# Performance work log

Measured on AMD Instinct MI355X. Metric: run time of the kernel, lower is better.

Reference implementation:

```python
import jax, jax.numpy as jnp
import numpy as np

D_MODEL = 1024
N_HEADS = 16
D_Q = 64
D_V = 64
N_SEG = 16
EPS_LN = 1e-5
EPS_MEM = 1e-6


def setup_inputs() -> dict:
    key = jax.random.key(0)
    ks = jax.random.split(key, 10)
    N, T = 4, 4096
    inp = {
        "query_sequences": jax.random.normal(ks[0], (N, T, D_MODEL), dtype=jnp.float32),
        "key_sequences": jax.random.normal(ks[1], (N, T, D_MODEL), dtype=jnp.float32),
        "value_sequences": jax.random.normal(ks[2], (N, T, D_MODEL), dtype=jnp.float32),
        "Wq": jax.random.normal(ks[3], (D_MODEL, N_HEADS * D_Q), dtype=jnp.float32) * 0.02,
        "Wk": jax.random.normal(ks[4], (D_MODEL, N_HEADS * D_Q), dtype=jnp.float32) * 0.02,
        "Wv": jax.random.normal(ks[5], (D_MODEL, N_HEADS * D_V), dtype=jnp.float32) * 0.02,
        "Wo": jax.random.normal(ks[6], (N_HEADS * D_V, D_MODEL), dtype=jnp.float32) * 0.02,
        "ln_w": jnp.ones((D_MODEL,), dtype=jnp.float32),
        "ln_b": jnp.zeros((D_MODEL,), dtype=jnp.float32),
        "beta": jnp.ones((1,), dtype=jnp.float32),
    }
    return inp


def _layer_norm(x, w, b):
    mu = jnp.mean(x, axis=-1, keepdims=True)
    var = jnp.var(x, axis=-1, keepdims=True)
    return (x - mu) * jax.lax.rsqrt(var + EPS_LN) * w + b


def reference(query_sequences, key_sequences, value_sequences, Wq, Wk, Wv, Wo, ln_w, ln_b, beta):
    N, t, _ = query_sequences.shape
    S = t // N_SEG  # segment length (256)

    # qkv_norm applied to q, and (self-attention) to k and v as well
    qn = _layer_norm(query_sequences, ln_w, ln_b)
    kn = _layer_norm(key_sequences, ln_w, ln_b)
    vn = _layer_norm(value_sequences, ln_w, ln_b)

    # project and split heads -> [N, H, t, d]
    qh = (qn @ Wq).reshape(N, t, N_HEADS, D_Q).transpose(0, 2, 1, 3)
    kh = (kn @ Wk).reshape(N, t, N_HEADS, D_Q).transpose(0, 2, 1, 3)
    vh = (vn @ Wv).reshape(N, t, N_HEADS, D_V).transpose(0, 2, 1, 3)

    # segment: [N_SEG, N, H, S, d] so lax.scan iterates segments sequentially
    seg = lambda x, d: x.reshape(N, N_HEADS, N_SEG, S, d).transpose(2, 0, 1, 3, 4)
    q_segs, k_segs, v_segs = seg(qh, D_Q), seg(kh, D_Q), seg(vh, D_V)

    b_gate = jax.nn.sigmoid(beta)[0]            # scalar mixing gate
    scale = 1.0 / np.sqrt(D_Q).astype(np.float32)
    causal = jnp.tril(jnp.ones((S, S), dtype=bool))

    def step(carry, xs):
        mem, z = carry                          # [N,H,Dq,Dv], [N,H,Dq]
        qs, ks_, vs = xs                        # [N,H,S,d]
        sq = jax.nn.elu(qs) + 1.0
        sk = jax.nn.elu(ks_) + 1.0
        # retrieve from compressive memory
        num = jnp.einsum('nhsd,nhde->nhse', sq, mem)
        den = jnp.einsum('nhsd,nhd->nhs', sq, z)[..., None] + EPS_MEM
        a_mem = num / den                       # [N,H,S,Dv]
        # local causal softmax attention within the segment
        scores = jnp.einsum('nhsd,nhtd->nhst', qs, ks_) * scale
        scores = jnp.where(causal, scores, -jnp.inf)
        probs = jax.nn.softmax(scores, axis=-1)
        attn = jnp.einsum('nhst,nhtd->nhsd', probs, vs)
        out = b_gate * a_mem + (1.0 - b_gate) * attn
        # linear memory update
        mem = mem + jnp.einsum('nhsd,nhse->nhde', sk, vs)
        z = z + sk.sum(axis=2)
        return (mem, z), out

    mem0 = jnp.zeros((N, N_HEADS, D_Q, D_V), dtype=query_sequences.dtype)
    z0 = jnp.zeros((N, N_HEADS, D_Q), dtype=query_sequences.dtype)
    _, outs = jax.lax.scan(step, (mem0, z0), (q_segs, k_segs, v_segs))

    # outs: [N_SEG, N, H, S, Dv] -> [N, t, H*Dv]
    seqs = outs.transpose(1, 0, 3, 2, 4).reshape(N, t, N_HEADS * D_V)
    return seqs @ Wo
```

## Files before the change

kernel.cpp:

```cpp
#include <hip/hip_runtime.h>
#include <stdint.h>
#include <math.h>


typedef __attribute__((ext_vector_type(8))) short bf16x8_t;
typedef __attribute__((ext_vector_type(4))) short short4_t;
typedef __attribute__((ext_vector_type(4))) float f32x4;

__device__ __forceinline__ float bf2f(short s){
  union { unsigned u; float f; } v; v.u = ((unsigned)(unsigned short)s) << 16; return v.f;
}
__device__ __forceinline__ short f2bf(float f){
  union { float fl; unsigned u; } v; v.fl = f;
  unsigned r = v.u + 0x7FFFu + ((v.u >> 16) & 1u);
  return (short)(unsigned short)(r >> 16);
}
__device__ __forceinline__ f32x4 mfma16(bf16x8_t a, bf16x8_t b, f32x4 c){
  return __builtin_amdgcn_mfma_f32_16x16x32_bf16(a, b, c, 0, 0, 0);
}
__device__ __forceinline__ void gl_lds16(const short* g, short* l){
  __builtin_amdgcn_global_load_lds((const __attribute__((address_space(1))) void*)g,
                                   (__attribute__((address_space(3))) void*)l, 16, 0, 0);
}

__global__ __launch_bounds__(256) void ln3(const float* __restrict__ xq, const float* __restrict__ xk,
                                           const float* __restrict__ xv,
                                           const float* __restrict__ gw, const float* __restrict__ gb,
                                           short* __restrict__ oq, short* __restrict__ ok,
                                           short* __restrict__ ov){
  const int row = blockIdx.x, which = blockIdx.y, tid = threadIdx.x;
  const float* x = which == 0 ? xq : which == 1 ? xk : xv;
  short* out     = which == 0 ? oq : which == 1 ? ok : ov;
  const float4 v = *reinterpret_cast<const float4*>(x + (size_t)row*1024 + tid*4);
  float s  = v.x + v.y + v.z + v.w;
  float s2 = v.x*v.x + v.y*v.y + v.z*v.z + v.w*v.w;
  #pragma unroll
  for (int off = 1; off < 64; off <<= 1){
    s  += __shfl_xor(s,  off);
    s2 += __shfl_xor(s2, off);
  }
  __shared__ float red[8];
  if ((tid & 63) == 0){ red[tid>>6] = s; red[4 + (tid>>6)] = s2; }
  __syncthreads();
  s  = red[0] + red[1] + red[2] + red[3];
  s2 = red[4] + red[5] + red[6] + red[7];
  const float mu  = s * (1.0f/1024.0f);
  const float var = s2 * (1.0f/1024.0f) - mu*mu;
  const float rs  = rsqrtf(var + 1e-5f);
  const float4 wv = *reinterpret_cast<const float4*>(gw + tid*4);
  const float4 bv = *reinterpret_cast<const float4*>(gb + tid*4);
  short4_t o;
  o[0] = f2bf((v.x-mu)*rs*wv.x + bv.x);
  o[1] = f2bf((v.y-mu)*rs*wv.y + bv.y);
  o[2] = f2bf((v.z-mu)*rs*wv.z + bv.z);
  o[3] = f2bf((v.w-mu)*rs*wv.w + bv.w);
  *reinterpret_cast<short4_t*>(out + (size_t)row*1024 + tid*4) = o;
}

__global__ __launch_bounds__(256) void wcast4(const float* __restrict__ W0, const float* __restrict__ W1,
                                              const float* __restrict__ W2, const float* __restrict__ W3,
                                              short* __restrict__ T0, short* __restrict__ T1,
                                              short* __restrict__ T2, short* __restrict__ T3){
  const int z = blockIdx.z;
  const float* W = z == 0 ? W0 : z == 1 ? W1 : z == 2 ? W2 : W3;
  short* Wt      = z == 0 ? T0 : z == 1 ? T1 : z == 2 ? T2 : T3;
  __shared__ float tile[64][65];
  const int bx = blockIdx.x, by = blockIdx.y, tid = threadIdx.x;
  #pragma unroll
  for (int p=0;p<4;++p){
    int idx = p*256 + tid;
    int r = idx >> 4, c4 = (idx & 15) << 2;
    const float4 v = *reinterpret_cast<const float4*>(W + (size_t)(by*64 + r)*1024 + bx*64 + c4);
    tile[r][c4+0] = v.x; tile[r][c4+1] = v.y; tile[r][c4+2] = v.z; tile[r][c4+3] = v.w;
  }
  __syncthreads();
  #pragma unroll
  for (int p=0;p<4;++p){
    int idx = p*256 + tid;
    int r = idx >> 4, c4 = (idx & 15) << 2;
    short4_t o;
    o[0] = f2bf(tile[c4+0][r]); o[1] = f2bf(tile[c4+1][r]);
    o[2] = f2bf(tile[c4+2][r]); o[3] = f2bf(tile[c4+3][r]);
    *reinterpret_cast<short4_t*>(Wt + (size_t)(bx*64 + r)*1024 + by*64 + c4) = o;
  }
}

__device__ __forceinline__ void remap_mc(int n, int& m0, int& c0){
  int xcd = n & 7, idx = n >> 3;
  m0 = ((xcd << 3) + (idx & 7)) << 8;
  c0 = (idx >> 3) << 8;
}

__device__ __forceinline__ void gemm_body(short* smem, const short* __restrict__ A,
                                          const short* __restrict__ Bt, void* __restrict__ C,
                                          int mode, int m0, int c0){
  short* As = smem;
  short* Bs = smem + 32768;
  const int tid = threadIdx.x;
  const int lane = tid & 63, wid = tid >> 6;
  const int wr = wid >> 2, wc = wid & 3;
  const int l15 = lane & 15, lhi = lane >> 4;

  const short* Asrc[4]; const short* Bsrc[4];
  #pragma unroll
  for (int p=0;p<4;++p){
    int i = tid + 512*p;
    int r = i >> 3, g = (i & 7) ^ (r & 7);
    Asrc[p] = A  + (size_t)(m0 + r)*1024 + g*8;
    Bsrc[p] = Bt + (size_t)(c0 + r)*1024 + g*8;
  }

  f32x4 acc[8][4];
  #pragma unroll
  for (int m=0;m<8;++m)
    #pragma unroll
    for (int n=0;n<4;++n) acc[m][n] = (f32x4){0.f,0.f,0.f,0.f};

  #define STAGE_A0(t) { short* _d=&As[((t)&1)<<14]; int _k=(t)<<6; \
      gl_lds16(Asrc[0]+_k, _d+tid*8); gl_lds16(Asrc[1]+_k, _d+4096+tid*8); }
  #define STAGE_A1(t) { short* _d=&As[((t)&1)<<14]; int _k=(t)<<6; \
      gl_lds16(Asrc[2]+_k, _d+8192+tid*8); gl_lds16(Asrc[3]+_k, _d+12288+tid*8); }
  #define STAGE_B0(t) { short* _d=&Bs[((t)&1)<<14]; int _k=(t)<<6; \
      gl_lds16(Bsrc[0]+_k, _d+tid*8); gl_lds16(Bsrc[1]+_k, _d+4096+tid*8); }
  #define STAGE_B1(t) { short* _d=&Bs[((t)&1)<<14]; int _k=(t)<<6; \
      gl_lds16(Bsrc[2]+_k, _d+8192+tid*8); gl_lds16(Bsrc[3]+_k, _d+12288+tid*8); }

  STAGE_B0(0); STAGE_A0(0); STAGE_B1(0); STAGE_A1(0);
  STAGE_B0(1); STAGE_A0(1);
  asm volatile("s_waitcnt vmcnt(4)" ::: "memory");
  __builtin_amdgcn_s_barrier();

  for (int t = 0; t < 16; ++t){
    const short* Ab = &As[(t & 1) << 14];
    const short* Bb = &Bs[(t & 1) << 14];
    bf16x8_t af[4][2], bfr[4][2];
    #pragma unroll
    for (int m=0;m<4;++m){
      int r = wr*128 + m*16 + l15;
      #pragma unroll
      for (int ks=0;ks<2;++ks){
        int sl = (ks*4 + lhi) ^ (r & 7);
        af[m][ks] = *reinterpret_cast<const bf16x8_t*>(&Ab[r*64 + sl*8]);
      }
    }
    #pragma unroll
    for (int n=0;n<2;++n){
      int r = wc*64 + n*16 + l15;
      #pragma unroll
      for (int ks=0;ks<2;++ks){
        int sl = (ks*4 + lhi) ^ (r & 7);
        bfr[n][ks] = *reinterpret_cast<const bf16x8_t*>(&Bb[r*64 + sl*8]);
      }
    }
    if (t < 15) STAGE_B1(t+1);
    __builtin_amdgcn_s_setprio(1);
    #pragma unroll
    for (int m=0;m<4;++m)
      #pragma unroll
      for (int n=0;n<2;++n)
        #pragma unroll
        for (int ks=0;ks<2;++ks)
          acc[m][n] = mfma16(af[m][ks], bfr[n][ks], acc[m][n]);
    __builtin_amdgcn_s_setprio(0);
    #pragma unroll
    for (int n=2;n<4;++n){
      int r = wc*64 + n*16 + l15;
      #pragma unroll
      for (int ks=0;ks<2;++ks){
        int sl = (ks*4 + lhi) ^ (r & 7);
        bfr[n][ks] = *reinterpret_cast<const bf16x8_t*>(&Bb[r*64 + sl*8]);
      }
    }
    if (t < 15) STAGE_A1(t+1);
    __builtin_amdgcn_s_setprio(1);
    #pragma unroll
    for (int m=0;m<4;++m)
      #pragma unroll
      for (int n=2;n<4;++n)
        #pragma unroll
        for (int ks=0;ks<2;++ks)
          acc[m][n] = mfma16(af[m][ks], bfr[n][ks], acc[m][n]);
    __builtin_amdgcn_s_setprio(0);
    asm volatile("" ::: "memory");
    __builtin_amdgcn_s_barrier();
    asm volatile("" ::: "memory");
    #pragma unroll
    for (int m=0;m<4;++m){
      int r = wr*128 + 64 + m*16 + l15;
      #pragma unroll
      for (int ks=0;ks<2;++ks){
        int sl = (ks*4 + lhi) ^ (r & 7);
        af[m][ks] = *reinterpret_cast<const bf16x8_t*>(&Ab[r*64 + sl*8]);
      }
    }
    if (t < 14) STAGE_B0(t+2);
    __builtin_amdgcn_s_setprio(1);
    #pragma unroll
    for (int m=0;m<4;++m)
      #pragma unroll
      for (int n=0;n<2;++n)
        #pragma unroll
        for (int ks=0;ks<2;++ks)
          acc[4+m][n] = mfma16(af[m][ks], bfr[n][ks], acc[4+m][n]);
    __builtin_amdgcn_s_setprio(0);
    asm volatile("" ::: "memory");
    __builtin_amdgcn_s_barrier();
    asm volatile("" ::: "memory");
    if (t < 14) STAGE_A0(t+2);
    __builtin_amdgcn_s_setprio(1);
    #pragma unroll
    for (int m=0;m<4;++m)
      #pragma unroll
      for (int n=2;n<4;++n)
        #pragma unroll
        for (int ks=0;ks<2;++ks)
          acc[4+m][n] = mfma16(af[m][ks], bfr[n][ks], acc[4+m][n]);
    __builtin_amdgcn_s_setprio(0);
    if (t < 14)       { asm volatile("s_waitcnt vmcnt(4)" ::: "memory"); }
    else if (t == 14) { asm volatile("s_waitcnt vmcnt(0)" ::: "memory"); }
    if (t < 15) __builtin_amdgcn_s_barrier();
  }
  #undef STAGE_A0
  #undef STAGE_A1
  #undef STAGE_B0
  #undef STAGE_B1

  if (mode == 0){
    short* Cb = (short*)C;
    #pragma unroll
    for (int m=0;m<8;++m)
      #pragma unroll
      for (int n=0;n<4;++n)
        #pragma unroll
        for (int j=0;j<4;++j){
          int row = m0 + wr*128 + m*16 + lhi*4 + j;
          int col = c0 + wc*64 + n*16 + l15;
          size_t oidx = ((size_t)((row>>12)*16 + (col>>6)) * 4096 + (size_t)(row & 4095)) * 64 + (col & 63);
          Cb[oidx] = f2bf(acc[m][n][j]);
        }
  } else if (mode == 2){
    short* Cb = (short*)C;
    #pragma unroll
    for (int m=0;m<8;++m)
      #pragma unroll
      for (int n=0;n<4;++n){
        int rowb = m0 + wr*128 + m*16 + lhi*4;
        int col  = c0 + wc*64 + n*16 + l15;
        int nh = ((rowb>>12)<<4) + (col>>6);
        int e  = col & 63;
        int tt = rowb & 4095;
        short4_t o;
        #pragma unroll
        for (int j=0;j<4;++j) o[j] = f2bf(acc[m][n][j]);
        *reinterpret_cast<short4_t*>(&Cb[((size_t)nh*64 + e)*4096 + tt]) = o;
      }
  } else {
    float* Cf = (float*)C;
    #pragma unroll
    for (int m=0;m<8;++m)
      #pragma unroll
      for (int n=0;n<4;++n)
        #pragma unroll
        for (int j=0;j<4;++j){
          int row = m0 + wr*128 + m*16 + lhi*4 + j;
          int col = c0 + wc*64 + n*16 + l15;
          Cf[(size_t)row*1024 + col] = acc[m][n][j];
        }
  }
}

__global__ __launch_bounds__(512, 2) void gemm_qkv(const short* __restrict__ A0, const short* __restrict__ A1,
    const short* __restrict__ A2, const short* __restrict__ B0, const short* __restrict__ B1,
    const short* __restrict__ B2, short* __restrict__ C0, short* __restrict__ C1, short* __restrict__ C2){
  extern __shared__ short smem[];
  const int z = blockIdx.z;
  const short* A = z == 0 ? A0 : z == 1 ? A1 : A2;
  const short* B = z == 0 ? B0 : z == 1 ? B1 : B2;
  short* C       = z == 0 ? C0 : z == 1 ? C1 : C2;
  int m0, c0; remap_mc(blockIdx.x + 64*blockIdx.y, m0, c0);
  gemm_body(smem, A, B, (void*)C, z == 2 ? 2 : 0, m0, c0);
}

__global__ __launch_bounds__(512, 2) void gemm_wo(const short* __restrict__ A, const short* __restrict__ Bt,
                                                  float* __restrict__ C){
  extern __shared__ short smem[];
  int m0, c0; remap_mc(blockIdx.x + 64*blockIdx.y, m0, c0);
  gemm_body(smem, A, Bt, (void*)C, 1, m0, c0);
}

__global__ __launch_bounds__(256) void stageA(const short* __restrict__ kh, const short* __restrict__ vhT,
                                              short* __restrict__ delta_b, float* __restrict__ zd){
  const int seg = blockIdx.x, nh = blockIdx.y, tid = threadIdx.x;
  const int lane = tid & 63, w = tid >> 6;
  const int l15 = lane & 15, lhi = lane >> 4;
  __shared__ short skT[64*256];
  const size_t thead = (size_t)nh*4096 + (size_t)seg*256;

  #pragma unroll
  for (int ch=0; ch<8; ++ch){
    int s  = ch*32 + (tid>>3);
    int lc = (tid&7)*8;
    bf16x8_t kv = *reinterpret_cast<const bf16x8_t*>(kh + (thead + s)*64 + lc);
    #pragma unroll
    for (int j=0;j<8;++j){
      float f = bf2f(kv[j]);
      short sv = f2bf((f > 0.f) ? (f + 1.f) : __expf(f));
      int d = lc + j;
      int bo = ((d*256 + s) << 1) ^ (((d>>3)&7) << 4);
      *reinterpret_cast<short*>(reinterpret_cast<char*>(skT) + bo) = sv;
    }
  }
  __syncthreads();

  bf16x8_t ones;
  #pragma unroll
  for (int i=0;i<8;++i) ones[i] = (short)0x3F80;

  f32x4 dacc[4], zacc[4];
  #pragma unroll
  for (int jf=0;jf<4;++jf){ dacc[jf] = (f32x4){0.f,0.f,0.f,0.f}; zacc[jf] = (f32x4){0.f,0.f,0.f,0.f}; }

  #pragma unroll
  for (int ks=0; ks<8; ++ks){
    bf16x8_t av = *reinterpret_cast<const bf16x8_t*>(
        vhT + ((size_t)nh*64 + w*16 + l15)*4096 + (size_t)seg*256 + ks*32 + lhi*8);
    #pragma unroll
    for (int jf=0;jf<4;++jf){
      int d  = jf*16 + l15;
      int so = ks*32 + lhi*8;
      int bo = ((d*256 + so) << 1) ^ (((d>>3)&7) << 4);
      bf16x8_t bk = *reinterpret_cast<const bf16x8_t*>(reinterpret_cast<char*>(skT) + bo);
      dacc[jf] = mfma16(av, bk, dacc[jf]);
      if (w == 0) zacc[jf] = mfma16(ones, bk, zacc[jf]);
    }
  }

  short* dp = delta_b + (size_t)(seg*64 + nh)*4096;
  #pragma unroll
  for (int jf=0;jf<4;++jf)
    #pragma unroll
    for (int j=0;j<4;++j)
      dp[(w*16 + lhi*4 + j)*64 + jf*16 + l15] = f2bf(dacc[jf][j]);
  if (w == 0 && lhi == 0){
    #pragma unroll
    for (int jf=0;jf<4;++jf)
      zd[(size_t)(seg*64 + nh)*64 + jf*16 + l15] = zacc[jf][0];
  }
}

__global__ __launch_bounds__(256) void stageB(const short* __restrict__ delta_b, const float* __restrict__ zd,
                                              short* __restrict__ mpre_b, float* __restrict__ zpre){
  const int c = blockIdx.x, nh = blockIdx.y, tid = threadIdx.x;
  const int idx = c*256 + tid;
  float acc = 0.f;
  for (int seg=0; seg<16; ++seg){
    size_t b = (size_t)(seg*64 + nh)*4096 + idx;
    mpre_b[b] = f2bf(acc);
    acc += bf2f(delta_b[b]);
  }
  if (c == 0 && tid < 64){
    float za = 0.f;
    for (int seg=0; seg<16; ++seg){
      size_t zb = (size_t)(seg*64 + nh)*64 + tid;
      zpre[zb] = za;
      za += zd[zb];
    }
  }
}

__global__ __launch_bounds__(256) void stageC(const short* __restrict__ qh, const short* __restrict__ kh,
    const short* __restrict__ vhT, const short* __restrict__ mpre_b, const float* __restrict__ z_pre,
    const float* __restrict__ beta, short* __restrict__ seqs)
{
  const int seg  = blockIdx.x;
  const int nh   = blockIdx.y;
  const int tid = threadIdx.x;
  const int lane = tid & 63, w = tid >> 6;
  const int l15 = lane & 15, lhi = lane >> 4;

  __shared__ short Ks[2][4096];
  __shared__ short Vs[2][4096];
  __shared__ float zl[64];
  __shared__ short pl[4][64][72];

  const size_t thead = (size_t)nh*4096 + (size_t)seg*256;

  const short* Ksrc[2]; const short* Vsrc[2];
  #pragma unroll
  for (int p=0;p<2;++p){
    int i = tid + 256*p, r = i >> 3, g = (i & 7) ^ (r & 7);
    Ksrc[p] = kh + (thead + r)*64 + g*8;
    Vsrc[p] = vhT + ((size_t)nh*64 + r)*4096 + (size_t)seg*256 + g*8;
  }
  #define STAGE_KV(kt) { short* _kd = Ks[(kt)&1]; short* _vd = Vs[(kt)&1]; \
      gl_lds16(Ksrc[0] + (kt)*4096, _kd + tid*8); \
      gl_lds16(Ksrc[1] + (kt)*4096, _kd + 2048 + tid*8); \
      gl_lds16(Vsrc[0] + (kt)*64,  _vd + tid*8); \
      gl_lds16(Vsrc[1] + (kt)*64,  _vd + 2048 + tid*8); }

  if (tid < 64) zl[tid] = z_pre[(size_t)(seg*64 + nh)*64 + tid];

  bf16x8_t aq[4][2];
  #pragma unroll
  for (int m=0;m<4;++m)
    #pragma unroll
    for (int ks=0;ks<2;++ks)
      aq[m][ks] = *reinterpret_cast<const bf16x8_t*>(qh + (thead + w*64 + m*16 + l15)*64 + ks*32 + lhi*8);

  STAGE_KV(0);
  asm volatile("s_waitcnt vmcnt(0)" ::: "memory");
  __syncthreads();

  const float bg = 1.f / (1.f + __expf(-beta[0]));
  const float scale = 0.125f;
  bf16x8_t ones;
  #pragma unroll
  for (int i=0;i<8;++i) ones[i] = (short)0x3F80;

  f32x4 o_acc[4][4], l_acc[4];
  #pragma unroll
  for (int m=0;m<4;++m){
    l_acc[m] = (f32x4){0.f,0.f,0.f,0.f};
    #pragma unroll
    for (int jf=0;jf<4;++jf) o_acc[m][jf] = (f32x4){0.f,0.f,0.f,0.f};
  }

  for (int kt = 0; kt < 4; ++kt){
    const short* Kb = Ks[kt & 1];
    const short* Vb = Vs[kt & 1];
    if (kt < 3) STAGE_KV(kt+1);
    if (kt <= w){
      f32x4 s_acc[4][4];
      #pragma unroll
      for (int m=0;m<4;++m)
        #pragma unroll
        for (int jf=0;jf<4;++jf) s_acc[m][jf] = (f32x4){0.f,0.f,0.f,0.f};
      #pragma unroll
      for (int ks=0;ks<2;++ks){
        bf16x8_t bk[4];
        #pragma unroll
        for (int jf=0;jf<4;++jf){
          int r = jf*16 + l15;
          int sl = (ks*4 + lhi) ^ (r & 7);
          bk[jf] = *reinterpret_cast<const bf16x8_t*>(&Kb[r*64 + sl*8]);
        }
        #pragma unroll
        for (int m=0;m<4;++m)
          #pragma unroll
          for (int jf=0;jf<4;++jf)
            s_acc[m][jf] = mfma16(aq[m][ks], bk[jf], s_acc[m][jf]);
      }
      const bool diag = (kt == w);
      #pragma unroll
      for (int m=0;m<4;++m)
        #pragma unroll
        for (int jf=0;jf<4;++jf)
          #pragma unroll
          for (int j=0;j<4;++j){
            float vv = s_acc[m][jf][j] * scale;
            if (diag){
              int sr = (w<<6) + m*16 + lhi*4 + j;
              int tc = (kt<<6) + jf*16 + l15;
              if (tc > sr) vv = -INFINITY;
            }
            float pv = __expf(vv);
            pl[w][m*16 + lhi*4 + j][jf*16 + l15] = f2bf(pv);
          }
      #pragma unroll
      for (int ks2=0;ks2<2;++ks2){
        bf16x8_t ap[4], bv[4];
        #pragma unroll
        for (int m=0;m<4;++m)
          ap[m] = *reinterpret_cast<const bf16x8_t*>(&pl[w][m*16 + l15][ks2*32 + lhi*8]);
        #pragma unroll
        for (int jf=0;jf<4;++jf){
          int e = jf*16 + l15;
          int sl = (ks2*4 + lhi) ^ (e & 7);
          bv[jf] = *reinterpret_cast<const bf16x8_t*>(&Vb[e*64 + sl*8]);
        }
        #pragma unroll
        for (int m=0;m<4;++m){
          l_acc[m] = mfma16(ap[m], ones, l_acc[m]);
          #pragma unroll
          for (int jf=0;jf<4;++jf)
            o_acc[m][jf] = mfma16(ap[m], bv[jf], o_acc[m][jf]);
        }
      }
    }
    if (kt < 3){
      asm volatile("s_waitcnt vmcnt(0)" ::: "memory");
      __builtin_amdgcn_s_barrier();
    }
  }
  #undef STAGE_KV

  bf16x8_t sq[4][2];
  #pragma unroll
  for (int m=0;m<4;++m)
    #pragma unroll
    for (int ks=0;ks<2;++ks)
      #pragma unroll
      for (int i=0;i<8;++i){
        float f = bf2f(aq[m][ks][i]);
        sq[m][ks][i] = f2bf((f > 0.f) ? (f + 1.f) : __expf(f));
      }
  bf16x8_t bz[2];
  #pragma unroll
  for (int ks=0;ks<2;++ks)
    #pragma unroll
    for (int i=0;i<8;++i) bz[ks][i] = f2bf(zl[ks*32 + lhi*8 + i]);

  const short* mpbase = mpre_b + (size_t)(seg*64 + nh)*4096;
  f32x4 n_acc[4][4], d_acc[4];
  #pragma unroll
  for (int m=0;m<4;++m){
    d_acc[m] = (f32x4){0.f,0.f,0.f,0.f};
    #pragma unroll
    for (int jf=0;jf<4;++jf) n_acc[m][jf] = (f32x4){0.f,0.f,0.f,0.f};
  }
  #pragma unroll
  for (int ks=0;ks<2;++ks){
    bf16x8_t bm[4];
    #pragma unroll
    for (int jf=0;jf<4;++jf)
      bm[jf] = *reinterpret_cast<const bf16x8_t*>(mpbase + (jf*16 + l15)*64 + ks*32 + lhi*8);
    #pragma unroll
    for (int m=0;m<4;++m){
      #pragma unroll
      for (int jf=0;jf<4;++jf) n_acc[m][jf] = mfma16(sq[m][ks], bm[jf], n_acc[m][jf]);
      d_acc[m] = mfma16(sq[m][ks], bz[ks], d_acc[m]);
    }
  }

  const int nb = nh >> 4, hh = nh & 15;
  #pragma unroll
  for (int m=0;m<4;++m)
    #pragma unroll
    for (int jf=0;jf<4;++jf)
      #pragma unroll
      for (int j=0;j<4;++j){
        float attn = o_acc[m][jf][j] / l_acc[m][j];
        float amem = n_acc[m][jf][j] / (d_acc[m][j] + 1e-6f);
        float ov = bg*amem + (1.f-bg)*attn;
        int srow = (w<<6) + m*16 + lhi*4 + j;
        seqs[((size_t)nb*4096 + (size_t)seg*256 + srow)*1024 + hh*64 + jf*16 + l15] = f2bf(ov);
      }
}

extern "C" void kernel_launch(void* const* d_in, const int* in_sizes, int n_in,
                              void* d_out, int out_size, void* d_ws, size_t ws_size,
                              hipStream_t stream){
  (void)in_sizes; (void)n_in; (void)out_size; (void)ws_size;
  const float* q    = (const float*)d_in[0];
  const float* k    = (const float*)d_in[1];
  const float* v    = (const float*)d_in[2];
  const float* Wq   = (const float*)d_in[3];
  const float* Wk   = (const float*)d_in[4];
  const float* Wv   = (const float*)d_in[5];
  const float* Wo   = (const float*)d_in[6];
  const float* lnw  = (const float*)d_in[7];
  const float* lnb  = (const float*)d_in[8];
  const float* beta = (const float*)d_in[9];
  char* ws = (char*)d_ws;
  const size_t MB = 1024ull*1024ull;
  short* WqT    = (short*)(ws + 0*MB);
  short* WkT    = (short*)(ws + 2*MB);
  short* WvT    = (short*)(ws + 4*MB);
  short* WoT    = (short*)(ws + 6*MB);
  short* xn_v   = (short*)(ws + 8*MB);
  short* seqs   = xn_v;
  short* qh     = (short*)(ws + 40*MB);
  short* kh     = (short*)(ws + 72*MB);
  short* vhT    = (short*)(ws + 104*MB);
  short* delta_b= (short*)(ws + 136*MB);
  float* zd     = (float*)(ws + 144*MB);
  short* mpre_b = (short*)(ws + 145*MB);
  float* zpre   = (float*)(ws + 153*MB);
  short* xn_q   = (short*)d_out;
  short* xn_k   = (short*)d_out + 16384ull*1024ull;

  wcast4<<<dim3(16,16,4),256,0,stream>>>(Wq,Wk,Wv,Wo, WqT,WkT,WvT,WoT);
  ln3<<<dim3(16384,3),256,0,stream>>>(q,k,v, lnw,lnb, xn_q,xn_k,xn_v);

  const size_t lds_gemm = 131072;
  gemm_qkv<<<dim3(64,4,3),512,lds_gemm,stream>>>(xn_q,xn_k,xn_v, WqT,WkT,WvT, qh,kh,vhT);

  stageA<<<dim3(16,64),256,0,stream>>>(kh, vhT, delta_b, zd);
  stageB<<<dim3(16,64),256,0,stream>>>(delta_b, zd, mpre_b, zpre);
  stageC<<<dim3(16,64),256,0,stream>>>(qh, kh, vhT, mpre_b, zpre, beta, seqs);
  gemm_wo<<<dim3(64,4),512,lds_gemm,stream>>>(seqs, WoT, (float*)d_out);
}
```

Baseline: 307.9 us.

## Interleave query rows across waves to balance causal attention work

The local attention kernel now gives each wave strided 16-row slices (m*64 + w*16) instead of one contiguous 64-row block. Every wave then does a similar amount of causal work per key tile, rather than wave 3 doing four tiles while wave 0 does one. The kt loop is fully unrolled with compile-time masking of the skipped m-blocks. The GEMM and attention barriers also gain sched_barrier fences so the compiler cannot move instructions across s_barrier, at some cost in scheduling freedom.

```diff
diff --git a/kernel.cpp b/kernel.cpp
--- a/kernel.cpp
+++ b/kernel.cpp
@@ -129,6 +129,8 @@
   STAGE_B0(1); STAGE_A0(1);
   asm volatile("s_waitcnt vmcnt(4)" ::: "memory");
   __builtin_amdgcn_s_barrier();
+  __builtin_amdgcn_sched_barrier(0);
+  asm volatile("" ::: "memory");
 
   for (int t = 0; t < 16; ++t){
     const short* Ab = &As[(t & 1) << 14];
@@ -183,6 +185,7 @@
     __builtin_amdgcn_s_setprio(0);
     asm volatile("" ::: "memory");
     __builtin_amdgcn_s_barrier();
+    __builtin_amdgcn_sched_barrier(0);
     asm volatile("" ::: "memory");
     #pragma unroll
     for (int m=0;m<4;++m){
@@ -205,6 +208,7 @@
     __builtin_amdgcn_s_setprio(0);
     asm volatile("" ::: "memory");
     __builtin_amdgcn_s_barrier();
+    __builtin_amdgcn_sched_barrier(0);
     asm volatile("" ::: "memory");
     if (t < 14) STAGE_A0(t+2);
     __builtin_amdgcn_s_setprio(1);
@@ -218,7 +222,11 @@
     __builtin_amdgcn_s_setprio(0);
     if (t < 14)       { asm volatile("s_waitcnt vmcnt(4)" ::: "memory"); }
     else if (t == 14) { asm volatile("s_waitcnt vmcnt(0)" ::: "memory"); }
-    if (t < 15) __builtin_amdgcn_s_barrier();
+    if (t < 15){
+      __builtin_amdgcn_s_barrier();
+      __builtin_amdgcn_sched_barrier(0);
+      asm volatile("" ::: "memory");
+    }
   }
   #undef STAGE_A0
   #undef STAGE_A1
@@ -405,7 +413,7 @@
   for (int m=0;m<4;++m)
     #pragma unroll
     for (int ks=0;ks<2;++ks)
-      aq[m][ks] = *reinterpret_cast<const bf16x8_t*>(qh + (thead + w*64 + m*16 + l15)*64 + ks*32 + lhi*8);
+      aq[m][ks] = *reinterpret_cast<const bf16x8_t*>(qh + (thead + m*64 + w*16 + l15)*64 + ks*32 + lhi*8);
 
   STAGE_KV(0);
   asm volatile("s_waitcnt vmcnt(0)" ::: "memory");
@@ -425,71 +433,73 @@
     for (int jf=0;jf<4;++jf) o_acc[m][jf] = (f32x4){0.f,0.f,0.f,0.f};
   }
 
+  #pragma unroll
   for (int kt = 0; kt < 4; ++kt){
     const short* Kb = Ks[kt & 1];
     const short* Vb = Vs[kt & 1];
     if (kt < 3) STAGE_KV(kt+1);
-    if (kt <= w){
-      f32x4 s_acc[4][4];
+    f32x4 s_acc[4][4];
+    #pragma unroll
+    for (int m=0;m<4;++m)
+      if (m >= kt)
+        #pragma unroll
+        for (int jf=0;jf<4;++jf) s_acc[m][jf] = (f32x4){0.f,0.f,0.f,0.f};
+    #pragma unroll
+    for (int ks=0;ks<2;++ks){
+      bf16x8_t bk[4];
+      #pragma unroll
+      for (int jf=0;jf<4;++jf){
+        int r = jf*16 + l15;
+        int sl = (ks*4 + lhi) ^ (r & 7);
+        bk[jf] = *reinterpret_cast<const bf16x8_t*>(&Kb[r*64 + sl*8]);
+      }
       #pragma unroll
       for (int m=0;m<4;++m)
-        #pragma unroll
-        for (int jf=0;jf<4;++jf) s_acc[m][jf] = (f32x4){0.f,0.f,0.f,0.f};
-      #pragma unroll
-      for (int ks=0;ks<2;++ks){
-        bf16x8_t bk[4];
-        #pragma unroll
-        for (int jf=0;jf<4;++jf){
-          int r = jf*16 + l15;
-          int sl = (ks*4 + lhi) ^ (r & 7);
-          bk[jf] = *reinterpret_cast<const bf16x8_t*>(&Kb[r*64 + sl*8]);
-        }
-        #pragma unroll
-        for (int m=0;m<4;++m)
+        if (m >= kt)
           #pragma unroll
           for (int jf=0;jf<4;++jf)
             s_acc[m][jf] = mfma16(aq[m][ks], bk[jf], s_acc[m][jf]);
-      }
-      const bool diag = (kt == w);
-      #pragma unroll
-      for (int m=0;m<4;++m)
+    }
+    #pragma unroll
+    for (int m=0;m<4;++m)
+      if (m >= kt)
         #pragma unroll
         for (int jf=0;jf<4;++jf)
           #pragma unroll
           for (int j=0;j<4;++j){
             float vv = s_acc[m][jf][j] * scale;
-            if (diag){
-              int sr = (w<<6) + m*16 + lhi*4 + j;
-              int tc = (kt<<6) + jf*16 + l15;
+            if (m == kt){
+              int sr = w*16 + lhi*4 + j;
+              int tc = jf*16 + l15;
               if (tc > sr) vv = -INFINITY;
             }
             float pv = __expf(vv);
             pl[w][m*16 + lhi*4 + j][jf*16 + l15] = f2bf(pv);
           }
-      #pragma unroll
-      for (int ks2=0;ks2<2;++ks2){
-        bf16x8_t ap[4], bv[4];
-        #pragma unroll
-        for (int m=0;m<4;++m)
-          ap[m] = *reinterpret_cast<const bf16x8_t*>(&pl[w][m*16 + l15][ks2*32 + lhi*8]);
-        #pragma unroll
-        for (int jf=0;jf<4;++jf){
-          int e = jf*16 + l15;
-          int sl = (ks2*4 + lhi) ^ (e & 7);
-          bv[jf] = *reinterpret_cast<const bf16x8_t*>(&Vb[e*64 + sl*8]);
-        }
-        #pragma unroll
-        for (int m=0;m<4;++m){
-          l_acc[m] = mfma16(ap[m], ones, l_acc[m]);
+    #pragma unroll
+    for (int ks2=0;ks2<2;++ks2){
+      bf16x8_t bv[4];
+      #pragma unroll
+      for (int jf=0;jf<4;++jf){
+        int e = jf*16 + l15;
+        int sl = (ks2*4 + lhi) ^ (e & 7);
+        bv[jf] = *reinterpret_cast<const bf16x8_t*>(&Vb[e*64 + sl*8]);
+      }
+      #pragma unroll
+      for (int m=0;m<4;++m)
+        if (m >= kt){
+          bf16x8_t ap = *reinterpret_cast<const bf16x8_t*>(&pl[w][m*16 + l15][ks2*32 + lhi*8]);
+          l_acc[m] = mfma16(ap, ones, l_acc[m]);
           #pragma unroll
           for (int jf=0;jf<4;++jf)
-            o_acc[m][jf] = mfma16(ap[m], bv[jf], o_acc[m][jf]);
+            o_acc[m][jf] = mfma16(ap, bv[jf], o_acc[m][jf]);
         }
-      }
     }
     if (kt < 3){
       asm volatile("s_waitcnt vmcnt(0)" ::: "memory");
       __builtin_amdgcn_s_barrier();
+      __builtin_amdgcn_sched_barrier(0);
+      asm volatile("" ::: "memory");
     }
   }
   #undef STAGE_KV
@@ -542,7 +552,7 @@
         float attn = o_acc[m][jf][j] / l_acc[m][j];
         float amem = n_acc[m][jf][j] / (d_acc[m][j] + 1e-6f);
         float ov = bg*amem + (1.f-bg)*attn;
-        int srow = (w<<6) + m*16 + lhi*4 + j;
+        int srow = m*64 + w*16 + lhi*4 + j;
         seqs[((size_t)nb*4096 + (size_t)seg*256 + srow)*1024 + hh*64 + jf*16 + l15] = f2bf(ov);
       }
 }
```

After: 292.6 us. 1.05x faster.
